# Performance work log

Measured on AMD Instinct MI355X. Metric: run time of the kernel, lower is better.

The kernel has to match this reference:

```python
import jax, jax.numpy as jnp
import numpy as np

FP8_E4M3_MAX = 448.0  # matches the 448.0 constant in the torch module


def setup_inputs() -> dict:
    key = jax.random.key(0)
    kx, kw, kb = jax.random.split(key, 3)
    B, S, D_IN, D_OUT = 4, 2048, 4096, 4096
    x = jax.random.normal(kx, (B, S, D_IN), dtype=jnp.float32)
    # Simulate the __init__-time FP8 quantization of the linear weight.
    w = jax.random.normal(kw, (D_OUT, D_IN), dtype=jnp.float32) * 0.02
    amax = jnp.max(jnp.abs(w))
    weight_scale = FP8_E4M3_MAX / (amax + 1e-12)
    weight_fp8 = (w * weight_scale).astype(jnp.float8_e4m3fn)  # stored FP8 buffer
    weight_inv_scale = (1.0 / weight_scale).astype(jnp.float32)
    bias = jax.random.normal(kb, (D_OUT,), dtype=jnp.float32) * 0.02
    return {"x": x, "weight_fp8": weight_fp8,
            "weight_inv_scale": weight_inv_scale, "bias": bias}


def reference(x, weight_fp8, weight_inv_scale, bias):
    # forward: dequantize FP8 weight to compute dtype, scale, then dense linear
    w = weight_fp8.astype(x.dtype) * weight_inv_scale.astype(x.dtype)  # [D_OUT, D_IN]
    # F.linear(x, w, bias) == x @ w.T + bias
    return jnp.einsum('bsd,od->bso', x, w) + bias.astype(x.dtype)
```

## Files before the change

### kernel.cpp

```cpp
#include <hip/hip_runtime.h>
#include <hip/hip_bf16.h>
#include <stdint.h>
#include <stddef.h>

typedef __bf16 bf16x8 __attribute__((ext_vector_type(8)));
typedef float  f32x4  __attribute__((ext_vector_type(4)));

__device__ __forceinline__ float fp8e4m3_to_f32(uint32_t b) {
    uint32_t e = (b >> 3) & 15u, m = b & 7u;
    float mag;
    if (e == 0)
        mag = (float)m * (1.0f / 512.0f);
    else
        mag = __uint_as_float(((e + 120u) << 23) | (m << 20));
    return (b & 0x80u) ? -mag : mag;
}

__device__ __forceinline__ unsigned short f32_to_bf16_bits(float f) {
    uint32_t x = __float_as_uint(f);
    uint32_t r = x + 0x7fffu + ((x >> 16) & 1u);
    return (unsigned short)(r >> 16);
}

__device__ __forceinline__ void gload_lds16(const void* g, void* l) {
    __builtin_amdgcn_global_load_lds(
        (const __attribute__((address_space(1))) uint32_t*)g,
        (__attribute__((address_space(3))) uint32_t*)l,
        16, 0, 0);
}

__global__ void detect_kernel(const uint32_t* __restrict__ w,
                              uint32_t* __restrict__ flag) {
    __shared__ int sF, sB;
    if (threadIdx.x == 0) { sF = 1; sB = 1; }
    __syncthreads();
    int f32ok = 1, bf16ok = 1;
    #pragma unroll
    for (int i = 0; i < 16; ++i) {
        uint32_t u = w[threadIdx.x * 16 + i];
        if (u & 0x000FFFFFu) f32ok = 0;
        if (u & 0x000F000Fu) bf16ok = 0;
    }
    if (!f32ok)  atomicExch(&sF, 0);
    if (!bf16ok) atomicExch(&sB, 0);
    __syncthreads();
    if (threadIdx.x == 0)
        *flag = sF ? 0u : (sB ? 1u : 2u);
}

__global__ void cvt_x_kernel(const float* __restrict__ x,
                             unsigned short* __restrict__ out, size_t n8) {
    size_t stride = (size_t)gridDim.x * blockDim.x;
    for (size_t i = (size_t)blockIdx.x * blockDim.x + threadIdx.x; i < n8; i += stride) {
        const float4* p = (const float4*)(x + i * 8);
        float4 a = p[0], b = p[1];
        union { uint4 v; unsigned short s[8]; } o;
        o.s[0] = f32_to_bf16_bits(a.x); o.s[1] = f32_to_bf16_bits(a.y);
        o.s[2] = f32_to_bf16_bits(a.z); o.s[3] = f32_to_bf16_bits(a.w);
        o.s[4] = f32_to_bf16_bits(b.x); o.s[5] = f32_to_bf16_bits(b.y);
        o.s[6] = f32_to_bf16_bits(b.z); o.s[7] = f32_to_bf16_bits(b.w);
        *(uint4*)(out + i * 8) = o.v;
    }
}

__global__ void prep_w_kernel(const void* __restrict__ wsrc,
                              const uint32_t* __restrict__ flag,
                              unsigned short* __restrict__ out, size_t n8) {
    const uint32_t mode = *flag;
    size_t stride = (size_t)gridDim.x * blockDim.x;
    for (size_t i = (size_t)blockIdx.x * blockDim.x + threadIdx.x; i < n8; i += stride) {
        union { uint4 v; unsigned short s[8]; } o;
        if (mode == 0) {
            const float4* p = (const float4*)((const float*)wsrc + i * 8);
            float4 a = p[0], b = p[1];
            o.s[0] = f32_to_bf16_bits(a.x); o.s[1] = f32_to_bf16_bits(a.y);
            o.s[2] = f32_to_bf16_bits(a.z); o.s[3] = f32_to_bf16_bits(a.w);
            o.s[4] = f32_to_bf16_bits(b.x); o.s[5] = f32_to_bf16_bits(b.y);
            o.s[6] = f32_to_bf16_bits(b.z); o.s[7] = f32_to_bf16_bits(b.w);
        } else if (mode == 1) {
            o.v = *(const uint4*)((const unsigned short*)wsrc + i * 8);
        } else {
            union { uint2 v; uint8_t b[8]; } u;
            u.v = *(const uint2*)((const uint8_t*)wsrc + i * 8);
            #pragma unroll
            for (int j = 0; j < 8; ++j)
                o.s[j] = f32_to_bf16_bits(fp8e4m3_to_f32(u.b[j]));
        }
        *(uint4*)(out + i * 8) = o.v;
    }
}


#define GBM 256
#define GBN 256
#define GBK 64

#define LDA_(qm) do {                                                          \
    _Pragma("unroll") for (int m = 0; m < 4; ++m) {                            \
        AF[m][0] = *(const bf16x8*)(ldsA + aoff0 + ((qm)*8192 + m*2048));      \
        AF[m][1] = *(const bf16x8*)(ldsA + aoff1 + ((qm)*8192 + m*2048));      \
    }                                                                          \
} while (0)

#define LDB_(qn, Bf) do {                                                      \
    _Pragma("unroll") for (int n = 0; n < 2; ++n) {                            \
        Bf[n][0] = *(const bf16x8*)(ldsB + boff0 + ((qn)*4096 + n*2048));      \
        Bf[n][1] = *(const bf16x8*)(ldsB + boff1 + ((qn)*4096 + n*2048));      \
    }                                                                          \
} while (0)

#define MFMA_(qm, qn, Bf) do {                                                 \
    __builtin_amdgcn_s_setprio(1);                                             \
    _Pragma("unroll") for (int m = 0; m < 4; ++m)                              \
    _Pragma("unroll") for (int n = 0; n < 2; ++n)                              \
    _Pragma("unroll") for (int ks = 0; ks < 2; ++ks)                           \
        acc[(qm)*4+m][(qn)*2+n] = __builtin_amdgcn_mfma_f32_16x16x32_bf16(     \
            AF[m][ks], Bf[n][ks], acc[(qm)*4+m][(qn)*2+n], 0, 0, 0);           \
    __builtin_amdgcn_s_setprio(0);                                             \
} while (0)

#define STAGE_(gsrc, koff, ldst) do {                                          \
    const uint8_t* _p = (gsrc) + (koff);                                       \
    _Pragma("unroll") for (int j = 0; j < 4; ++j)                              \
        gload_lds16(_p + (size_t)j * 64 * KB2, (ldst) + (sdst + j*8192));      \
} while (0)

__global__ __launch_bounds__(512, 2)
void gemm256_sl(const unsigned short* __restrict__ A,
                const unsigned short* __restrict__ Bw,
                const float* __restrict__ invp,
                const float* __restrict__ bias,
                float* __restrict__ C, int M, int N, int K) {
    __shared__ unsigned short lds[2][2][GBM * GBK];
    char* ldsb = (char*)&lds[0][0][0];

    const size_t KB2 = (size_t)K * 2;
    const int KT = K / GBK;

    const int nwg = gridDim.x;
    const int b   = blockIdx.x;
    const int wg  = (b & 7) * (nwg >> 3) + (b >> 3);
    const int MT  = M / GBM;
    const int tm  = wg % MT;
    const int tn  = wg / MT;

    const int t     = threadIdx.x;
    const int lane  = t & 63;
    const int wid   = t >> 6;
    const int wm    = wid >> 2;
    const int wn    = wid & 3;
    const int laneQ = lane & 15;
    const int laneH = lane >> 4;
    const int xorv  = (laneQ & 7) << 4;
    const int lrow  = lane >> 3;
    const int lcb   = (lane & 7) ^ lrow;

    const int col0  = (0   + laneH * 16) ^ xorv;
    const int col1  = (64  + laneH * 16) ^ xorv;
    const int aoff0 = wm * 16384 + laneQ * 128 + col0;
    const int aoff1 = wm * 16384 + laneQ * 128 + col1;
    const int boff0 = wn * 8192  + laneQ * 128 + col0;
    const int boff1 = wn * 8192  + laneQ * 128 + col1;
    const int sdst  = wid * 1024 + lane * 16;

    const uint8_t* gA = (const uint8_t*)A +
        ((size_t)tm * GBM + wid * 8 + lrow) * KB2 + (size_t)lcb * 16;
    const uint8_t* gB = (const uint8_t*)Bw +
        ((size_t)tn * GBN + wid * 8 + lrow) * KB2 + (size_t)lcb * 16;

    f32x4 acc[8][4] = {};
    bf16x8 AF[4][2], B0[2][2], B1[2][2];

    STAGE_(gB, (size_t)0,   ldsb + 32768);
    STAGE_(gA, (size_t)0,   ldsb);
    STAGE_(gB, (size_t)128, ldsb + 65536 + 32768);
    STAGE_(gA, (size_t)128, ldsb + 65536);
    asm volatile("s_waitcnt vmcnt(8)" ::: "memory");
    __builtin_amdgcn_s_barrier();

    for (int kt = 0; kt < KT; ++kt) {
        const int coff = (kt & 1) << 16;
        const char* ldsA = ldsb + coff;
        const char* ldsB = ldsb + coff + 32768;
        char* ldsAw = (char*)ldsA;
        char* ldsBw = (char*)ldsB;
        const bool more = (kt + 2) < KT;
        const size_t kb2 = (size_t)(kt + 2) * 128;

        LDB_(0, B0);
        LDA_(0);
        MFMA_(0, 0, B0);
        LDB_(1, B1);
        MFMA_(0, 1, B1);
        LDA_(1);
        MFMA_(1, 0, B0);
        MFMA_(1, 1, B1);

        asm volatile("s_waitcnt lgkmcnt(0)" ::: "memory");
        __builtin_amdgcn_s_barrier();

        if (more) {
            STAGE_(gB, kb2, ldsBw);
            STAGE_(gA, kb2, ldsAw);
        }
        if (more) asm volatile("s_waitcnt vmcnt(8)" ::: "memory");
        else      asm volatile("s_waitcnt vmcnt(0)" ::: "memory");
        __builtin_amdgcn_s_barrier();
    }

    const float inv = *invp;
    float bv[4];
    #pragma unroll
    for (int n = 0; n < 4; ++n)
        bv[n] = bias[tn * GBN + wn * 64 + n * 16 + laneQ];

    #pragma unroll
    for (int m = 0; m < 8; ++m) {
        int rowb = tm * GBM + wm * 128 + m * 16 + laneH * 4;
        #pragma unroll
        for (int j = 0; j < 4; ++j) {
            float* cp = C + (size_t)(rowb + j) * N + tn * GBN + wn * 64;
            #pragma unroll
            for (int n = 0; n < 4; ++n)
                cp[n * 16 + laneQ] = acc[m][n][j] * inv + bv[n];
        }
    }
}

__global__ void naive_kernel(const float* __restrict__ x,
                             const void* __restrict__ wsrc,
                             const uint32_t* flag,
                             const float* __restrict__ invp,
                             const float* __restrict__ bias,
                             float* __restrict__ out, int M, int N, int K) {
    const uint32_t mode = flag ? *flag : 0u;
    size_t idx = (size_t)blockIdx.x * blockDim.x + threadIdx.x;
    if (idx >= (size_t)M * N) return;
    int m = (int)(idx / N), n = (int)(idx % N);
    const float* xr = x + (size_t)m * K;
    float s = 0.f;
    if (mode == 0) {
        const float* wr = (const float*)wsrc + (size_t)n * K;
        for (int k = 0; k < K; ++k) s += xr[k] * wr[k];
    } else if (mode == 1) {
        const unsigned short* wr = (const unsigned short*)wsrc + (size_t)n * K;
        for (int k = 0; k < K; ++k)
            s += xr[k] * __uint_as_float(((uint32_t)wr[k]) << 16);
    } else {
        const uint8_t* wr = (const uint8_t*)wsrc + (size_t)n * K;
        for (int k = 0; k < K; ++k) s += xr[k] * fp8e4m3_to_f32(wr[k]);
    }
    out[idx] = s * (*invp) + bias[n];
}

extern "C" void kernel_launch(void* const* d_in, const int* in_sizes, int n_in,
                              void* d_out, int out_size, void* d_ws, size_t ws_size,
                              hipStream_t stream) {
    const float*    x    = (const float*)d_in[0];
    const void*     wsrc = d_in[1];
    const float*    inv  = (const float*)d_in[2];
    const float*    bias = (const float*)d_in[3];
    float*          out  = (float*)d_out;

    const int K = in_sizes[1] / in_sizes[3];
    const int N = in_sizes[3];
    const int M = in_sizes[0] / K;

    const size_t needA = (size_t)M * K * sizeof(unsigned short);
    const size_t needB = (size_t)N * K * sizeof(unsigned short);

    const bool shape_ok = (M % GBM) == 0 && (N % GBN) == 0 && (K % GBK) == 0 &&
                          (K / GBK) >= 2 &&
                          (((M / GBM) * (N / GBN)) % 8) == 0;

    if (ws_size < needA + needB + 256 || !shape_ok) {
        size_t total = (size_t)M * N;
        uint32_t* flag = (ws_size >= 256) ? (uint32_t*)d_ws : nullptr;
        if (flag) detect_kernel<<<1, 256, 0, stream>>>((const uint32_t*)wsrc, flag);
        naive_kernel<<<(unsigned)((total + 255) / 256), 256, 0, stream>>>(
            x, wsrc, flag, inv, bias, out, M, N, K);
        return;
    }

    uint32_t*       flag = (uint32_t*)d_ws;
    unsigned short* Abf  = (unsigned short*)((char*)d_ws + 256);
    unsigned short* Wbf  = (unsigned short*)((char*)d_ws + 256 + needA);

    detect_kernel<<<1, 256, 0, stream>>>((const uint32_t*)wsrc, flag);
    cvt_x_kernel<<<2048, 256, 0, stream>>>(x, Abf, (size_t)M * K / 8);
    prep_w_kernel<<<2048, 256, 0, stream>>>(wsrc, flag, Wbf, (size_t)N * K / 8);

    dim3 grid((M / GBM) * (N / GBN));
    gemm256_sl<<<grid, 512, 0, stream>>>(Abf, Wbf, inv, bias, out, M, N, K);
}
```

Before: 311.0 us.

## Interleave half-tile global-to-LDS staging with MFMA phases in GEMM main loop

Restructures the K loop into four barrier-separated phases. Each phase issues half of the next A tile or the B tile two steps ahead, so global loads overlap with the MFMA groups instead of being issued in a block after compute. The A tile is now prefetched one stage ahead into the other buffer, while B stays two ahead but is written into the current buffer once its fragments have been read. The cost is many more workgroup barriers per iteration, and the tighter buffer reuse raises the risk of LDS races.

New measurement: 298.1 us. -4.2%, faster.

```diff
diff --git a/kernel.cpp b/kernel.cpp
--- a/kernel.cpp
+++ b/kernel.cpp
@@ -125,8 +125,17 @@
         gload_lds16(_p + (size_t)j * 64 * KB2, (ldst) + (sdst + j*8192));      \
 } while (0)
 
+#define STAGEH_(gsrc, koff, ldst, h) do {                                      \
+    const uint8_t* _p = (gsrc) + (koff);                                       \
+    _Pragma("unroll") for (int j = 2*(h); j < 2*(h) + 2; ++j)                  \
+        gload_lds16(_p + (size_t)j * 64 * KB2, (ldst) + (sdst + j*8192));      \
+} while (0)
+
+#define BAR_()   __builtin_amdgcn_s_barrier()
+#define LGKM0_() asm volatile("s_waitcnt lgkmcnt(0)" ::: "memory")
+
 __global__ __launch_bounds__(512, 2)
-void gemm256_sl(const unsigned short* __restrict__ A,
+void gemm256_p8(const unsigned short* __restrict__ A,
                 const unsigned short* __restrict__ Bw,
                 const float* __restrict__ invp,
                 const float* __restrict__ bias,
@@ -174,38 +183,46 @@
     STAGE_(gB, (size_t)0,   ldsb + 32768);
     STAGE_(gA, (size_t)0,   ldsb);
     STAGE_(gB, (size_t)128, ldsb + 65536 + 32768);
-    STAGE_(gA, (size_t)128, ldsb + 65536);
-    asm volatile("s_waitcnt vmcnt(8)" ::: "memory");
-    __builtin_amdgcn_s_barrier();
-
-    for (int kt = 0; kt < KT; ++kt) {
-        const int coff = (kt & 1) << 16;
-        const char* ldsA = ldsb + coff;
-        const char* ldsB = ldsb + coff + 32768;
-        char* ldsAw = (char*)ldsA;
-        char* ldsBw = (char*)ldsB;
-        const bool more = (kt + 2) < KT;
-        const size_t kb2 = (size_t)(kt + 2) * 128;
+    asm volatile("s_waitcnt vmcnt(4)" ::: "memory");
+    BAR_();
+
+    for (int j = 0; j < KT; ++j) {
+        const int p = (j & 1) << 16;
+        const char* ldsA = ldsb + p;
+        const char* ldsB = ldsb + p + 32768;
+        char* stA = ldsb + ((~j & 1) << 16);
+        char* stB = ldsb + p + 32768;
+        const bool pA = (j + 1) < KT;
+        const bool pB = (j + 2) < KT;
+        const size_t kA = (size_t)(j + 1) * 128;
+        const size_t kB = (size_t)(j + 2) * 128;
 
         LDB_(0, B0);
         LDA_(0);
+        if (pA) STAGEH_(gA, kA, stA, 0);
+        asm volatile("s_waitcnt lgkmcnt(8)" ::: "memory");
+        BAR_();  LGKM0_();
         MFMA_(0, 0, B0);
+        BAR_();
+
         LDB_(1, B1);
+        if (pA) STAGEH_(gA, kA, stA, 1);
+        BAR_();  LGKM0_();
         MFMA_(0, 1, B1);
+        BAR_();
+
         LDA_(1);
+        if (pB) STAGEH_(gB, kB, stB, 0);
+        BAR_();  LGKM0_();
+        MFMA_(1, 1, B1);
+        BAR_();
+
+        if (pB) STAGEH_(gB, kB, stB, 1);
+        BAR_();
         MFMA_(1, 0, B0);
-        MFMA_(1, 1, B1);
-
-        asm volatile("s_waitcnt lgkmcnt(0)" ::: "memory");
-        __builtin_amdgcn_s_barrier();
-
-        if (more) {
-            STAGE_(gB, kb2, ldsBw);
-            STAGE_(gA, kb2, ldsAw);
-        }
-        if (more) asm volatile("s_waitcnt vmcnt(8)" ::: "memory");
-        else      asm volatile("s_waitcnt vmcnt(0)" ::: "memory");
-        __builtin_amdgcn_s_barrier();
+        if (pB) asm volatile("s_waitcnt vmcnt(4)" ::: "memory");
+        else    asm volatile("s_waitcnt vmcnt(0)" ::: "memory");
+        BAR_();
     }
 
     const float inv = *invp;
@@ -291,5 +308,5 @@
     prep_w_kernel<<<2048, 256, 0, stream>>>(wsrc, flag, Wbf, (size_t)N * K / 8);
 
     dim3 grid((M / GBM) * (N / GBN));
-    gemm256_sl<<<grid, 512, 0, stream>>>(Abf, Wbf, inv, bias, out, M, N, K);
-}
+    gemm256_p8<<<grid, 512, 0, stream>>>(Abf, Wbf, inv, bias, out, M, N, K);
+}
```

## Use 4-wave 256x256 GEMM tile with 128x128 per-wave sub-tiles

Applied to the files above, without the earlier changes.

Restructures the GEMM workgroup from 8 waves (512 threads, 2 per CU) to 4 waves (256 threads, 1 per CU), so each wave computes a 128x128 output sub-tile instead of 128x64. All B fragments for the wave are loaded once per k-step and A fragments are streamed in pairs, which raises the MFMA-to-LDS-read ratio. Staging loads are remapped so each wave copies 64 rows. In exchange, accumulator register pressure doubles (256 VGPRs for acc), occupancy drops to one workgroup per CU, and there are fewer waves available to hide latency.

Result: slower. 321.1 us (+3.2%).

```diff
diff --git a/kernel.cpp b/kernel.cpp
--- a/kernel.cpp
+++ b/kernel.cpp
@@ -95,38 +95,38 @@
 #define GBN 256
 #define GBK 64
 
-#define LDA_(qm) do {                                                          \
-    _Pragma("unroll") for (int m = 0; m < 4; ++m) {                            \
-        AF[m][0] = *(const bf16x8*)(ldsA + aoff0 + ((qm)*8192 + m*2048));      \
-        AF[m][1] = *(const bf16x8*)(ldsA + aoff1 + ((qm)*8192 + m*2048));      \
+#define LDBALL_() do {                                                         \
+    _Pragma("unroll") for (int nt = 0; nt < 8; ++nt) {                         \
+        BF[nt][0] = *(const bf16x8*)(ldsB + boff0 + nt*2048);                  \
+        BF[nt][1] = *(const bf16x8*)(ldsB + boff1 + nt*2048);                  \
     }                                                                          \
 } while (0)
 
-#define LDB_(qn, Bf) do {                                                      \
-    _Pragma("unroll") for (int n = 0; n < 2; ++n) {                            \
-        Bf[n][0] = *(const bf16x8*)(ldsB + boff0 + ((qn)*4096 + n*2048));      \
-        Bf[n][1] = *(const bf16x8*)(ldsB + boff1 + ((qn)*4096 + n*2048));      \
+#define LDA2_(qa) do {                                                         \
+    _Pragma("unroll") for (int mt = 0; mt < 2; ++mt) {                         \
+        AF[mt][0] = *(const bf16x8*)(ldsA + aoff0 + ((qa)*2+mt)*2048);         \
+        AF[mt][1] = *(const bf16x8*)(ldsA + aoff1 + ((qa)*2+mt)*2048);         \
     }                                                                          \
 } while (0)
 
-#define MFMA_(qm, qn, Bf) do {                                                 \
+#define MFMA2_(qa) do {                                                        \
     __builtin_amdgcn_s_setprio(1);                                             \
-    _Pragma("unroll") for (int m = 0; m < 4; ++m)                              \
-    _Pragma("unroll") for (int n = 0; n < 2; ++n)                              \
+    _Pragma("unroll") for (int mt = 0; mt < 2; ++mt)                           \
+    _Pragma("unroll") for (int nt = 0; nt < 8; ++nt)                           \
     _Pragma("unroll") for (int ks = 0; ks < 2; ++ks)                           \
-        acc[(qm)*4+m][(qn)*2+n] = __builtin_amdgcn_mfma_f32_16x16x32_bf16(     \
-            AF[m][ks], Bf[n][ks], acc[(qm)*4+m][(qn)*2+n], 0, 0, 0);           \
+        acc[(qa)*2+mt][nt] = __builtin_amdgcn_mfma_f32_16x16x32_bf16(          \
+            AF[mt][ks], BF[nt][ks], acc[(qa)*2+mt][nt], 0, 0, 0);              \
     __builtin_amdgcn_s_setprio(0);                                             \
 } while (0)
 
 #define STAGE_(gsrc, koff, ldst) do {                                          \
     const uint8_t* _p = (gsrc) + (koff);                                       \
-    _Pragma("unroll") for (int j = 0; j < 4; ++j)                              \
-        gload_lds16(_p + (size_t)j * 64 * KB2, (ldst) + (sdst + j*8192));      \
-} while (0)
-
-__global__ __launch_bounds__(512, 2)
-void gemm256_sl(const unsigned short* __restrict__ A,
+    _Pragma("unroll") for (int j = 0; j < 8; ++j)                              \
+        gload_lds16(_p + (size_t)j * 8 * KB2, (ldst) + (sdst + j*1024));       \
+} while (0)
+
+__global__ __launch_bounds__(256, 1)
+void gemm256_w4(const unsigned short* __restrict__ A,
                 const unsigned short* __restrict__ Bw,
                 const float* __restrict__ invp,
                 const float* __restrict__ bias,
@@ -147,8 +147,8 @@
     const int t     = threadIdx.x;
     const int lane  = t & 63;
     const int wid   = t >> 6;
-    const int wm    = wid >> 2;
-    const int wn    = wid & 3;
+    const int wm    = wid >> 1;
+    const int wn    = wid & 1;
     const int laneQ = lane & 15;
     const int laneH = lane >> 4;
     const int xorv  = (laneQ & 7) << 4;
@@ -159,23 +159,23 @@
     const int col1  = (64  + laneH * 16) ^ xorv;
     const int aoff0 = wm * 16384 + laneQ * 128 + col0;
     const int aoff1 = wm * 16384 + laneQ * 128 + col1;
-    const int boff0 = wn * 8192  + laneQ * 128 + col0;
-    const int boff1 = wn * 8192  + laneQ * 128 + col1;
-    const int sdst  = wid * 1024 + lane * 16;
+    const int boff0 = wn * 16384 + laneQ * 128 + col0;
+    const int boff1 = wn * 16384 + laneQ * 128 + col1;
+    const int sdst  = wid * 8192 + lane * 16;
 
     const uint8_t* gA = (const uint8_t*)A +
-        ((size_t)tm * GBM + wid * 8 + lrow) * KB2 + (size_t)lcb * 16;
+        ((size_t)tm * GBM + wid * 64 + lrow) * KB2 + (size_t)lcb * 16;
     const uint8_t* gB = (const uint8_t*)Bw +
-        ((size_t)tn * GBN + wid * 8 + lrow) * KB2 + (size_t)lcb * 16;
-
-    f32x4 acc[8][4] = {};
-    bf16x8 AF[4][2], B0[2][2], B1[2][2];
+        ((size_t)tn * GBN + wid * 64 + lrow) * KB2 + (size_t)lcb * 16;
+
+    f32x4 acc[8][8] = {};
+    bf16x8 AF[2][2], BF[8][2];
 
     STAGE_(gB, (size_t)0,   ldsb + 32768);
     STAGE_(gA, (size_t)0,   ldsb);
     STAGE_(gB, (size_t)128, ldsb + 65536 + 32768);
     STAGE_(gA, (size_t)128, ldsb + 65536);
-    asm volatile("s_waitcnt vmcnt(8)" ::: "memory");
+    asm volatile("s_waitcnt vmcnt(16)" ::: "memory");
     __builtin_amdgcn_s_barrier();
 
     for (int kt = 0; kt < KT; ++kt) {
@@ -187,14 +187,11 @@
         const bool more = (kt + 2) < KT;
         const size_t kb2 = (size_t)(kt + 2) * 128;
 
-        LDB_(0, B0);
-        LDA_(0);
-        MFMA_(0, 0, B0);
-        LDB_(1, B1);
-        MFMA_(0, 1, B1);
-        LDA_(1);
-        MFMA_(1, 0, B0);
-        MFMA_(1, 1, B1);
+        LDBALL_();
+        LDA2_(0);  MFMA2_(0);
+        LDA2_(1);  MFMA2_(1);
+        LDA2_(2);  MFMA2_(2);
+        LDA2_(3);  MFMA2_(3);
 
         asm volatile("s_waitcnt lgkmcnt(0)" ::: "memory");
         __builtin_amdgcn_s_barrier();
@@ -203,25 +200,25 @@
             STAGE_(gB, kb2, ldsBw);
             STAGE_(gA, kb2, ldsAw);
         }
-        if (more) asm volatile("s_waitcnt vmcnt(8)" ::: "memory");
+        if (more) asm volatile("s_waitcnt vmcnt(16)" ::: "memory");
         else      asm volatile("s_waitcnt vmcnt(0)" ::: "memory");
         __builtin_amdgcn_s_barrier();
     }
 
     const float inv = *invp;
-    float bv[4];
+    float bv[8];
     #pragma unroll
-    for (int n = 0; n < 4; ++n)
-        bv[n] = bias[tn * GBN + wn * 64 + n * 16 + laneQ];
+    for (int n = 0; n < 8; ++n)
+        bv[n] = bias[tn * GBN + wn * 128 + n * 16 + laneQ];
 
     #pragma unroll
     for (int m = 0; m < 8; ++m) {
         int rowb = tm * GBM + wm * 128 + m * 16 + laneH * 4;
         #pragma unroll
         for (int j = 0; j < 4; ++j) {
-            float* cp = C + (size_t)(rowb + j) * N + tn * GBN + wn * 64;
+            float* cp = C + (size_t)(rowb + j) * N + tn * GBN + wn * 128;
             #pragma unroll
-            for (int n = 0; n < 4; ++n)
+            for (int n = 0; n < 8; ++n)
                 cp[n * 16 + laneQ] = acc[m][n][j] * inv + bv[n];
         }
     }
@@ -291,5 +288,5 @@
     prep_w_kernel<<<2048, 256, 0, stream>>>(wsrc, flag, Wbf, (size_t)N * K / 8);
 
     dim3 grid((M / GBM) * (N / GBN));
-    gemm256_sl<<<grid, 512, 0, stream>>>(Abf, Wbf, inv, bias, out, M, N, K);
-}
+    gemm256_w4<<<grid, 256, 0, stream>>>(Abf, Wbf, inv, bias, out, M, N, K);
+}
```
